# Optimization experiments

Measured on AMD Instinct MI355X. Metric: run time of the kernel, lower is better.

The kernel has to match this reference:

```python
import jax, jax.numpy as jnp
import numpy as np


def setup_inputs() -> dict:
    key = jax.random.key(0)
    k1, k2 = jax.random.split(key)
    B, N, D = 32, 4096, 768
    x = jax.random.normal(k1, (B, N + 1, D), dtype=jnp.float32)
    significance = jax.random.normal(k2, (B, N), dtype=jnp.float32)
    return {"x": x, "significance": significance, "keep_tokens": 1024}


def reference(x, significance, keep_tokens):
    # x: [B, N+1, D] with CLS at position 0; significance: [B, N]
    cls_token = x[:, :1, :]              # [B, 1, D]
    tokens = x[:, 1:, :]                 # [B, N, D]
    if keep_tokens >= tokens.shape[1]:
        return x
    # top-k significance per batch (sorted descending, matching torch.topk)
    _, topk_indices = jax.lax.top_k(significance, keep_tokens)  # [B, K]
    pooled_tokens = jnp.take_along_axis(tokens, topk_indices[:, :, None], axis=1)  # [B, K, D]
    return jnp.concatenate([cls_token, pooled_tokens], axis=1)  # [B, 1+K, D]
```

## Files before the change

### kernel.cpp

```cpp
#include <hip/hip_runtime.h>

constexpr int B    = 32;
constexpr int NTOK = 4096;
constexpr int D    = 768;
constexpr int K    = 1024;
constexpr int D4   = D / 4;
constexpr int SORT_THREADS = 1024;

__device__ __forceinline__ unsigned monotone_u32(float f) {
  unsigned u = __float_as_uint(f);
  return (u & 0x80000000u) ? ~u : (u | 0x80000000u);
}

__global__ __launch_bounds__(SORT_THREADS)
void topk_sort_kernel(const float* __restrict__ sig, int* __restrict__ idx_out) {
  __shared__ unsigned long long keys[NTOK];
  const int b = blockIdx.x;
  const float* s = sig + (size_t)b * NTOK;

  #pragma unroll
  for (int rep = 0; rep < NTOK / SORT_THREADS; ++rep) {
    int i = threadIdx.x + rep * SORT_THREADS;
    unsigned u = monotone_u32(s[i]);
    keys[i] = ((unsigned long long)(~u) << 32) | (unsigned)i;
  }
  __syncthreads();

  for (int k = 2; k <= NTOK; k <<= 1) {
    for (int j = k >> 1; j > 0; j >>= 1) {
      #pragma unroll
      for (int rep = 0; rep < NTOK / SORT_THREADS; ++rep) {
        int i = threadIdx.x + rep * SORT_THREADS;
        int ixj = i ^ j;
        if (ixj > i) {
          unsigned long long a = keys[i];
          unsigned long long c = keys[ixj];
          if ((a > c) == ((i & k) == 0)) { keys[i] = c; keys[ixj] = a; }
        }
      }
      __syncthreads();
    }
  }

  idx_out[b * K + threadIdx.x] = (int)(unsigned)(keys[threadIdx.x] & 0xffffffffu);
}

__global__ __launch_bounds__(D4)
void gather_kernel(const float4* __restrict__ x, const int* __restrict__ idx,
                   float4* __restrict__ out) {
  const int blk = blockIdx.x;
  const int b   = blk / (K + 1);
  const int r   = blk - b * (K + 1);
  int src_row = 0;
  if (r != 0) src_row = 1 + idx[b * K + (r - 1)];
  const size_t src = ((size_t)b * (NTOK + 1) + src_row) * D4 + threadIdx.x;
  const size_t dst = (size_t)blk * D4 + threadIdx.x;
  out[dst] = x[src];
}

extern "C" void kernel_launch(void* const* d_in, const int* in_sizes, int n_in,
                              void* d_out, int out_size, void* d_ws, size_t ws_size,
                              hipStream_t stream) {
  const float* x   = (const float*)d_in[0];
  const float* sig = (const float*)d_in[1];
  int*   idx = (int*)d_ws;
  float* out = (float*)d_out;

  topk_sort_kernel<<<B, SORT_THREADS, 0, stream>>>(sig, idx);
  gather_kernel<<<B * (K + 1), D4, 0, stream>>>(
      (const float4*)x, idx, (float4*)out);
}
```

Measured before the change: 530.8 us.

## Split bitonic top-k sort into multi-block chunk sort and merge kernels

Splits the per-batch 4096-element bitonic sort across several launches. Chunk sorts run 128 blocks of 1024 keys each, merge2048 runs 64 blocks, and a final 32-block merge emits the top-k indices, so more CUs work on the sort. The compare-exchange indexing now maps each thread directly to a pair, which removes the idle-half branch. The gather switches to nontemporal loads and stores. In exchange it adds two extra launches and a round trip of the keys through global workspace.

```diff
diff --git a/kernel.cpp b/kernel.cpp
--- a/kernel.cpp
+++ b/kernel.cpp
@@ -5,49 +5,103 @@
 constexpr int D    = 768;
 constexpr int K    = 1024;
 constexpr int D4   = D / 4;
-constexpr int SORT_THREADS = 1024;
+constexpr int CH   = 1024;
+
+typedef float vfloat4 __attribute__((ext_vector_type(4)));
 
 __device__ __forceinline__ unsigned monotone_u32(float f) {
   unsigned u = __float_as_uint(f);
   return (u & 0x80000000u) ? ~u : (u | 0x80000000u);
 }
 
-__global__ __launch_bounds__(SORT_THREADS)
-void topk_sort_kernel(const float* __restrict__ sig, int* __restrict__ idx_out) {
-  __shared__ unsigned long long keys[NTOK];
-  const int b = blockIdx.x;
-  const float* s = sig + (size_t)b * NTOK;
+__device__ __forceinline__ unsigned long long mkkey(float v, unsigned gidx) {
+  return ((unsigned long long)(~monotone_u32(v)) << 32) | gidx;
+}
+
+__global__ __launch_bounds__(512)
+void chunk_sort(const float* __restrict__ sig, unsigned long long* __restrict__ wsk) {
+  __shared__ unsigned long long keys[CH];
+  const int b = blockIdx.x >> 2, c = blockIdx.x & 3;
+  const float* s = sig + (size_t)b * NTOK + c * CH;
 
   #pragma unroll
-  for (int rep = 0; rep < NTOK / SORT_THREADS; ++rep) {
-    int i = threadIdx.x + rep * SORT_THREADS;
-    unsigned u = monotone_u32(s[i]);
-    keys[i] = ((unsigned long long)(~u) << 32) | (unsigned)i;
+  for (int rep = 0; rep < 2; ++rep) {
+    int i = threadIdx.x + rep * 512;
+    keys[i] = mkkey(s[i], c * CH + i);
   }
   __syncthreads();
 
-  for (int k = 2; k <= NTOK; k <<= 1) {
+  for (int k = 2; k <= CH; k <<= 1) {
     for (int j = k >> 1; j > 0; j >>= 1) {
-      #pragma unroll
-      for (int rep = 0; rep < NTOK / SORT_THREADS; ++rep) {
-        int i = threadIdx.x + rep * SORT_THREADS;
-        int ixj = i ^ j;
-        if (ixj > i) {
-          unsigned long long a = keys[i];
-          unsigned long long c = keys[ixj];
-          if ((a > c) == ((i & k) == 0)) { keys[i] = c; keys[ixj] = a; }
-        }
-      }
+      int p = threadIdx.x;
+      int i = ((p & ~(j - 1)) << 1) | (p & (j - 1));
+      int ig = (c << 10) | i;
+      bool dir = ((ig & k) == 0);
+      unsigned long long a = keys[i], d = keys[i | j];
+      if ((a > d) == dir) { keys[i] = d; keys[i | j] = a; }
       __syncthreads();
     }
   }
 
-  idx_out[b * K + threadIdx.x] = (int)(unsigned)(keys[threadIdx.x] & 0xffffffffu);
+  unsigned long long* o = wsk + (size_t)b * NTOK + c * CH;
+  #pragma unroll
+  for (int rep = 0; rep < 2; ++rep) {
+    int i = threadIdx.x + rep * 512;
+    o[i] = keys[i];
+  }
+}
+
+__global__ __launch_bounds__(1024)
+void merge2048(unsigned long long* __restrict__ wsk) {
+  __shared__ unsigned long long keys[2048];
+  const int b = blockIdx.x >> 1, h = blockIdx.x & 1;
+  unsigned long long* g = wsk + (size_t)b * NTOK + h * 2048;
+  keys[threadIdx.x]        = g[threadIdx.x];
+  keys[threadIdx.x + 1024] = g[threadIdx.x + 1024];
+  __syncthreads();
+
+  const bool dir = (h == 0);
+  for (int j = 1024; j > 0; j >>= 1) {
+    int p = threadIdx.x;
+    int i = ((p & ~(j - 1)) << 1) | (p & (j - 1));
+    unsigned long long a = keys[i], d = keys[i | j];
+    if ((a > d) == dir) { keys[i] = d; keys[i | j] = a; }
+    __syncthreads();
+  }
+
+  g[threadIdx.x]        = keys[threadIdx.x];
+  g[threadIdx.x + 1024] = keys[threadIdx.x + 1024];
+}
+
+__global__ __launch_bounds__(1024)
+void merge4096_emit(const unsigned long long* __restrict__ wsk, int* __restrict__ idx) {
+  __shared__ unsigned long long keys[NTOK];
+  const int b = blockIdx.x;
+  const unsigned long long* g = wsk + (size_t)b * NTOK;
+  #pragma unroll
+  for (int rep = 0; rep < 4; ++rep) {
+    int i = threadIdx.x + rep * 1024;
+    keys[i] = g[i];
+  }
+  __syncthreads();
+
+  for (int j = 2048; j > 0; j >>= 1) {
+    #pragma unroll
+    for (int rep = 0; rep < 2; ++rep) {
+      int p = threadIdx.x + rep * 1024;
+      int i = ((p & ~(j - 1)) << 1) | (p & (j - 1));
+      unsigned long long a = keys[i], d = keys[i | j];
+      if (a > d) { keys[i] = d; keys[i | j] = a; }
+    }
+    __syncthreads();
+  }
+
+  idx[b * K + threadIdx.x] = (int)(unsigned)(keys[threadIdx.x] & 0xffffffffu);
 }
 
 __global__ __launch_bounds__(D4)
-void gather_kernel(const float4* __restrict__ x, const int* __restrict__ idx,
-                   float4* __restrict__ out) {
+void gather_kernel(const vfloat4* __restrict__ x, const int* __restrict__ idx,
+                   vfloat4* __restrict__ out) {
   const int blk = blockIdx.x;
   const int b   = blk / (K + 1);
   const int r   = blk - b * (K + 1);
@@ -55,7 +109,8 @@
   if (r != 0) src_row = 1 + idx[b * K + (r - 1)];
   const size_t src = ((size_t)b * (NTOK + 1) + src_row) * D4 + threadIdx.x;
   const size_t dst = (size_t)blk * D4 + threadIdx.x;
-  out[dst] = x[src];
+  vfloat4 v = __builtin_nontemporal_load(&x[src]);
+  __builtin_nontemporal_store(v, &out[dst]);
 }
 
 extern "C" void kernel_launch(void* const* d_in, const int* in_sizes, int n_in,
@@ -63,10 +118,13 @@
                               hipStream_t stream) {
   const float* x   = (const float*)d_in[0];
   const float* sig = (const float*)d_in[1];
-  int*   idx = (int*)d_ws;
   float* out = (float*)d_out;
 
-  topk_sort_kernel<<<B, SORT_THREADS, 0, stream>>>(sig, idx);
-  gather_kernel<<<B * (K + 1), D4, 0, stream>>>(
-      (const float4*)x, idx, (float4*)out);
+  unsigned long long* wsk = (unsigned long long*)d_ws;
+  int* idx = (int*)((char*)d_ws + (size_t)B * NTOK * sizeof(unsigned long long));
+
+  chunk_sort   <<<B * 4, 512,  0, stream>>>(sig, wsk);
+  merge2048    <<<B * 2, 1024, 0, stream>>>(wsk);
+  merge4096_emit<<<B,    1024, 0, stream>>>(wsk, idx);
+  gather_kernel<<<B * (K + 1), D4, 0, stream>>>((const vfloat4*)x, idx, (vfloat4*)out);
 }
```

New measurement: 492.4 us. -7.2%, faster.
